# Performance work log

Measured on AMD Instinct MI355X. Metric: run time of the kernel, lower is better.

The kernel has to match this reference:

```python
import jax, jax.numpy as jnp
import numpy as np

B, T, NB, H = 1024, 128, 13, 128
T_IN = 64  # input_timesteps


def setup_inputs() -> dict:
    key = jax.random.key(0)
    ks = jax.random.split(key, 7)
    s = 1.0 / np.sqrt(H)
    return {
        "x": jax.random.normal(ks[0], (B, T, NB), dtype=jnp.float32),
        "W_ih": jax.random.normal(ks[1], (4 * H, NB), dtype=jnp.float32) * s,
        "W_hh": jax.random.normal(ks[2], (4 * H, H), dtype=jnp.float32) * s,
        "b_ih": jax.random.normal(ks[3], (4 * H,), dtype=jnp.float32) * s,
        "b_hh": jax.random.normal(ks[4], (4 * H,), dtype=jnp.float32) * s,
        "W_out": jax.random.normal(ks[5], (NB, H), dtype=jnp.float32) * s,
        "b_out": jax.random.normal(ks[6], (NB,), dtype=jnp.float32) * s,
    }


def _lstm_cell(x_t, h, c, W_ih, W_hh, b_ih, b_hh):
    # PyTorch nn.LSTM gate order: input, forget, cell(g), output
    gates = x_t @ W_ih.T + h @ W_hh.T + (b_ih + b_hh)  # [B, 4H]
    i, f, g, o = jnp.split(gates, 4, axis=-1)
    i = jax.nn.sigmoid(i)
    f = jax.nn.sigmoid(f)
    g = jnp.tanh(g)
    o = jax.nn.sigmoid(o)
    c_new = f * c + i * g
    h_new = o * jnp.tanh(c_new)
    return h_new, c_new


def reference(x, W_ih, W_hh, b_ih, b_hh, W_out, b_out):
    # forward_train with teacher_forcing=False, gp_enabled=False:
    # 1) teacher-fed LSTM over x[:, :T_IN]
    batch = x.shape[0]
    h0 = jnp.zeros((batch, H), dtype=x.dtype)
    c0 = jnp.zeros((batch, H), dtype=x.dtype)

    def step_teacher(carry, x_t):
        h, c = carry
        h, c = _lstm_cell(x_t, h, c, W_ih, W_hh, b_ih, b_hh)
        y = h @ W_out.T + b_out  # [B, NB]
        return (h, c), y

    (h, c), ys1 = jax.lax.scan(step_teacher, (h0, c0),
                               jnp.swapaxes(x[:, :T_IN], 0, 1))  # ys1: [T_IN, B, NB]

    remaining = T - T_IN - 1

    def step_auto(carry, _):
        h, c, inp = carry
        h, c = _lstm_cell(inp, h, c, W_ih, W_hh, b_ih, b_hh)
        y = h @ W_out.T + b_out
        return (h, c, y), y

    _, ys2 = jax.lax.scan(step_auto, (h, c, x[:, T_IN]), None, length=remaining)

    out = jnp.concatenate([
        x[:, 0:1],
        jnp.swapaxes(ys1, 0, 1),
        jnp.swapaxes(ys2, 0, 1),
    ], axis=1)  # [B, T, NB]
    return out
```

## Files before the change

### kernel.cpp

```cpp
#include <hip/hip_runtime.h>
#include <math.h>

#define BATCH 1024
#define TT    128
#define NBI   13
#define HH    128
#define T_INP 64
#define BB    4
#define NBLK  (BATCH/BB)

#define LOG2E 1.4426950408889634f
#define C2L   2.8853900817779268f
#define C4L   5.7707801635558537f

typedef _Float16 half8 __attribute__((ext_vector_type(8)));
typedef float    f32x4 __attribute__((ext_vector_type(4)));

__device__ __forceinline__ unsigned short f16b(float v) {
    return __builtin_bit_cast(unsigned short, (_Float16)v);
}
__device__ __forceinline__ float rcpf_(float x) { return __builtin_amdgcn_rcpf(x); }

#if __has_builtin(__builtin_amdgcn_exp2f)
__device__ __forceinline__ float exp2_(float x) { return __builtin_amdgcn_exp2f(x); }
#else
__device__ __forceinline__ float exp2_(float x) { return __expf(x * 0.6931471805599453f); }
#endif

__device__ __forceinline__ void barrier_lds() {
    asm volatile("s_waitcnt lgkmcnt(0)" ::: "memory");
    __builtin_amdgcn_sched_barrier(0);
    __builtin_amdgcn_s_barrier();
    __builtin_amdgcn_sched_barrier(0);
}

#define WS_WHH   0
#define WS_WHAT  131072
#define WS_WIHP  262144
#define WS_WOUT  294912
#define WS_BT    299008
#define WS_BA    301056

__global__ void fold_kernel(const float* __restrict__ W_ih,
                            const float* __restrict__ W_hh,
                            const float* __restrict__ b_ih,
                            const float* __restrict__ b_hh,
                            const float* __restrict__ W_out,
                            const float* __restrict__ b_out,
                            unsigned char* __restrict__ ws)
{
    const int j = blockIdx.x;
    const int k = threadIdx.x;
    unsigned short* whh16  = (unsigned short*)(ws + WS_WHH);
    unsigned short* what16 = (unsigned short*)(ws + WS_WHAT);
    unsigned short* wihp16 = (unsigned short*)(ws + WS_WIHP);
    unsigned short* wout16 = (unsigned short*)(ws + WS_WOUT);
    float* bias_t = (float*)(ws + WS_BT);
    float* bias_a = (float*)(ws + WS_BA);

    const int gate = j >> 7;
    const float sc = (gate == 2) ? (2.0f * LOG2E) : (-LOG2E);

    float whh = W_hh[j * HH + k];
    float acc = whh;
#pragma unroll
    for (int m = 0; m < NBI; ++m)
        acc += W_ih[j * NBI + m] * W_out[m * HH + k];
    whh16[j * HH + k]  = f16b(sc * whh);
    what16[j * HH + k] = f16b(sc * acc);

    if (k < 32) wihp16[j * 32 + k] = (k < NBI) ? f16b(sc * W_ih[j * NBI + k]) : (unsigned short)0;
    if (k == 0) {
        float bt = b_ih[j] + b_hh[j];
        bias_t[j] = sc * bt;
        float ba = bt;
#pragma unroll
        for (int m = 0; m < NBI; ++m) ba += W_ih[j * NBI + m] * b_out[m];
        bias_a[j] = sc * ba;
    }
    if (j < 16) wout16[j * HH + k] = (j < NBI) ? f16b(W_out[j * HH + k]) : (unsigned short)0;
}

#define MFMA16(A, B, C) __builtin_amdgcn_mfma_f32_16x16x32_f16((A), (B), (C), 0, 0, 0)

__global__ __launch_bounds__(512, 2)
void lstm_main(const float* __restrict__ x,
               const float* __restrict__ b_out,
               const unsigned char* __restrict__ ws,
               float* __restrict__ out)
{
    const int j  = threadIdx.x;
    const int w  = j >> 6;
    const int l  = j & 63;
    const int q  = l >> 4;
    const int cb = l & 15;
    const int bbase = blockIdx.x * BB;

    const unsigned short* whh16  = (const unsigned short*)(ws + WS_WHH);
    const unsigned short* what16 = (const unsigned short*)(ws + WS_WHAT);
    const unsigned short* wihp16 = (const unsigned short*)(ws + WS_WIHP);
    const unsigned short* wout16 = (const unsigned short*)(ws + WS_WOUT);
    const float* btfp = (const float*)(ws + WS_BT);
    const float* bafp = (const float*)(ws + WS_BA);

    __shared__ half8 h_s[2][16][16];
    __shared__ half8 x_s[2][4][16];
    __shared__ float g_sf[4 * 512];

    half8 wf[4][4];
    half8 wxf[4];
    half8 wof[4];
    f32x4 binit[4];
#pragma unroll
    for (int a = 0; a < 4; ++a) {
        const int row = 64 * w + 16 * a + cb;
#pragma unroll
        for (int kk = 0; kk < 4; ++kk)
            wf[a][kk] = *(const half8*)(whh16 + row * HH + 32 * kk + 8 * q);
        wxf[a] = *(const half8*)(wihp16 + row * 32 + 8 * q);
#pragma unroll
        for (int r = 0; r < 4; ++r)
            binit[a][r] = btfp[64 * w + 16 * a + 4 * q + r];
    }
    const bool projw = (w == 7);
#pragma unroll
    for (int kk = 0; kk < 4; ++kk)
        wof[kk] = *(const half8*)(wout16 + cb * HH + 32 * kk + 8 * q);

    f32x4 bo4;
#pragma unroll
    for (int r = 0; r < 4; ++r) {
        const int m = 4 * q + r;
        bo4[r] = (m < NBI) ? b_out[m] : 0.0f;
    }
    const f32x4 z4 = {0.f, 0.f, 0.f, 0.f};
    float* pob = out + (size_t)(bbase + (cb & 3)) * TT * NBI;

    const int uu = j & 127;
    const int ub = j >> 7;
    const float* gme = g_sf + ub * 512 + uu;

    const int  sid = j - 384;
    const bool stg = (sid >= 0) && (sid < 52);
    int s_b = 0, s_m = 0;
    const float* xp0 = x;
    float xa_h = 0.f;
    if (stg) { s_b = sid / 13; s_m = sid - 13 * s_b;
               xp0 = x + (size_t)(bbase + s_b) * TT * NBI + s_m; }

    ((half8*)h_s)[j] = (half8)(_Float16)0.0f;
    if (j < 128) ((half8*)x_s)[j] = (half8)(_Float16)0.0f;
    __syncthreads();
    if (stg) {
        float v = xp0[0];
        ((_Float16*)&x_s[0][s_m >> 3][s_b])[s_m & 7] = (_Float16)v;
        out[(size_t)(bbase + s_b) * TT * NBI + s_m] = v;
        xa_h = xp0[NBI];
    }
    __syncthreads();

    float c = 0.0f;
    int cur = 0;

    for (int t = 0; t <= T_INP; ++t) {
        const int nxt = cur ^ 1;

        float xa_p = 0.f;
        if (stg && t + 2 <= T_INP) xa_p = xp0[(t + 2) * NBI];

        half8 xf  = x_s[cur][q][cb];
        half8 hb0 = h_s[cur][q][cb];
        half8 hb1 = h_s[cur][4 + q][cb];
        half8 hb2 = h_s[cur][8 + q][cb];
        half8 hb3 = h_s[cur][12 + q][cb];

        f32x4 a0 = MFMA16(wxf[0], xf, binit[0]);
        f32x4 a1 = MFMA16(wxf[1], xf, binit[1]);
        f32x4 a2 = MFMA16(wxf[2], xf, binit[2]);
        f32x4 a3 = MFMA16(wxf[3], xf, binit[3]);
        a0 = MFMA16(wf[0][0], hb0, a0); a1 = MFMA16(wf[1][0], hb0, a1);
        a2 = MFMA16(wf[2][0], hb0, a2); a3 = MFMA16(wf[3][0], hb0, a3);
        a0 = MFMA16(wf[0][1], hb1, a0); a1 = MFMA16(wf[1][1], hb1, a1);
        a2 = MFMA16(wf[2][1], hb1, a2); a3 = MFMA16(wf[3][1], hb1, a3);
        a0 = MFMA16(wf[0][2], hb2, a0); a1 = MFMA16(wf[1][2], hb2, a1);
        a2 = MFMA16(wf[2][2], hb2, a2); a3 = MFMA16(wf[3][2], hb2, a3);
        a0 = MFMA16(wf[0][3], hb3, a0); a1 = MFMA16(wf[1][3], hb3, a1);
        a2 = MFMA16(wf[2][3], hb3, a2); a3 = MFMA16(wf[3][3], hb3, a3);

        f32x4 pacc = z4;
        if (projw) {
            pacc = MFMA16(wof[0], hb0, z4);
            pacc = MFMA16(wof[1], hb1, pacc);
            pacc = MFMA16(wof[2], hb2, pacc);
            pacc = MFMA16(wof[3], hb3, pacc);
        }

        if (cb < 4) {
            float* gb = g_sf + cb * 512 + 64 * w + 4 * q;
            *(f32x4*)(gb)      = a0;
            *(f32x4*)(gb + 16) = a1;
            *(f32x4*)(gb + 32) = a2;
            *(f32x4*)(gb + 48) = a3;
        }
        if (projw && t >= 1 && cb < 4) {
#pragma unroll
            for (int r = 0; r < 4; ++r) {
                const int m = 4 * q + r;
                if (m < NBI) pob[t * NBI + m] = pacc[r] + bo4[r];
            }
        }
        barrier_lds();

        {
            float gi = gme[0], gf = gme[128], gg = gme[256], go = gme[384];
            float ig = rcpf_(1.0f + exp2_(gi));
            float fg = rcpf_(1.0f + exp2_(gf));
            float rg = rcpf_(exp2_(gg) + 1.0f);
            float gp = C2L - C4L * rg;
            float og = rcpf_(1.0f + exp2_(go));
            float cn = fg * c + ig * gp;
            c = cn;
            float ec = exp2_(cn);
            float hv = og * (1.0f - 2.0f * rcpf_(ec + 1.0f));
            ((_Float16*)&h_s[nxt][uu >> 3][ub])[uu & 7] = (_Float16)hv;
        }
        if (stg && t + 1 <= T_INP) {
            ((_Float16*)&x_s[nxt][s_m >> 3][s_b])[s_m & 7] = (_Float16)xa_h;
            xa_h = xa_p;
        }
        barrier_lds();
        cur = nxt;
    }

#pragma unroll
    for (int a = 0; a < 4; ++a) {
        const int row = 64 * w + 16 * a + cb;
#pragma unroll
        for (int kk = 0; kk < 4; ++kk)
            wf[a][kk] = *(const half8*)(what16 + row * HH + 32 * kk + 8 * q);
#pragma unroll
        for (int r = 0; r < 4; ++r)
            binit[a][r] = bafp[64 * w + 16 * a + 4 * q + r];
    }

    for (int t = T_INP + 1; t < TT - 1; ++t) {
        const int nxt = cur ^ 1;

        half8 hb0 = h_s[cur][q][cb];
        half8 hb1 = h_s[cur][4 + q][cb];
        half8 hb2 = h_s[cur][8 + q][cb];
        half8 hb3 = h_s[cur][12 + q][cb];

        f32x4 a0 = MFMA16(wf[0][0], hb0, binit[0]);
        f32x4 a1 = MFMA16(wf[1][0], hb0, binit[1]);
        f32x4 a2 = MFMA16(wf[2][0], hb0, binit[2]);
        f32x4 a3 = MFMA16(wf[3][0], hb0, binit[3]);
        a0 = MFMA16(wf[0][1], hb1, a0); a1 = MFMA16(wf[1][1], hb1, a1);
        a2 = MFMA16(wf[2][1], hb1, a2); a3 = MFMA16(wf[3][1], hb1, a3);
        a0 = MFMA16(wf[0][2], hb2, a0); a1 = MFMA16(wf[1][2], hb2, a1);
        a2 = MFMA16(wf[2][2], hb2, a2); a3 = MFMA16(wf[3][2], hb2, a3);
        a0 = MFMA16(wf[0][3], hb3, a0); a1 = MFMA16(wf[1][3], hb3, a1);
        a2 = MFMA16(wf[2][3], hb3, a2); a3 = MFMA16(wf[3][3], hb3, a3);

        f32x4 pacc = z4;
        if (projw) {
            pacc = MFMA16(wof[0], hb0, z4);
            pacc = MFMA16(wof[1], hb1, pacc);
            pacc = MFMA16(wof[2], hb2, pacc);
            pacc = MFMA16(wof[3], hb3, pacc);
        }

        if (cb < 4) {
            float* gb = g_sf + cb * 512 + 64 * w + 4 * q;
            *(f32x4*)(gb)      = a0;
            *(f32x4*)(gb + 16) = a1;
            *(f32x4*)(gb + 32) = a2;
            *(f32x4*)(gb + 48) = a3;
        }
        if (projw && cb < 4) {
#pragma unroll
            for (int r = 0; r < 4; ++r) {
                const int m = 4 * q + r;
                if (m < NBI) pob[t * NBI + m] = pacc[r] + bo4[r];
            }
        }
        barrier_lds();

        {
            float gi = gme[0], gf = gme[128], gg = gme[256], go = gme[384];
            float ig = rcpf_(1.0f + exp2_(gi));
            float fg = rcpf_(1.0f + exp2_(gf));
            float rg = rcpf_(exp2_(gg) + 1.0f);
            float gp = C2L - C4L * rg;
            float og = rcpf_(1.0f + exp2_(go));
            float cn = fg * c + ig * gp;
            c = cn;
            float ec = exp2_(cn);
            float hv = og * (1.0f - 2.0f * rcpf_(ec + 1.0f));
            ((_Float16*)&h_s[nxt][uu >> 3][ub])[uu & 7] = (_Float16)hv;
        }
        barrier_lds();
        cur = nxt;
    }

    if (projw) {
        half8 hb0 = h_s[cur][q][cb];
        half8 hb1 = h_s[cur][4 + q][cb];
        half8 hb2 = h_s[cur][8 + q][cb];
        half8 hb3 = h_s[cur][12 + q][cb];
        f32x4 pacc = MFMA16(wof[0], hb0, z4);
        pacc = MFMA16(wof[1], hb1, pacc);
        pacc = MFMA16(wof[2], hb2, pacc);
        pacc = MFMA16(wof[3], hb3, pacc);
        if (cb < 4) {
#pragma unroll
            for (int r = 0; r < 4; ++r) {
                const int m = 4 * q + r;
                if (m < NBI) pob[(TT - 1) * NBI + m] = pacc[r] + bo4[r];
            }
        }
    }
}

extern "C" void kernel_launch(void* const* d_in, const int* in_sizes, int n_in,
                              void* d_out, int out_size, void* d_ws, size_t ws_size,
                              hipStream_t stream)
{
    const float* x     = (const float*)d_in[0];
    const float* W_ih  = (const float*)d_in[1];
    const float* W_hh  = (const float*)d_in[2];
    const float* b_ih  = (const float*)d_in[3];
    const float* b_hh  = (const float*)d_in[4];
    const float* W_out = (const float*)d_in[5];
    const float* b_out = (const float*)d_in[6];
    float* out = (float*)d_out;
    unsigned char* ws = (unsigned char*)d_ws;

    fold_kernel<<<512, HH, 0, stream>>>(W_ih, W_hh, b_ih, b_hh, W_out, b_out, ws);
    lstm_main<<<NBLK, 512, 0, stream>>>(x, b_out, ws, out);
}
```

Measured before the change: 179.9 us.

## Halve batch rows per block to double block count and occupancy

Each block now handles 2 batch rows instead of 4, so there are 512 blocks instead of 256, and launch bounds ask for 4 blocks per CU instead of 2. LDS arrays gain a padding column that all unused MFMA batch columns read from, and gate scratch rows are padded. Only the first 256 threads run the cell update. The aim is more parallelism across the 256 CUs on this latency-bound recurrence. The cost is that half of each MFMA's work is now wasted, and the tighter register budget from the higher occupancy target may cause spills, since each thread keeps about 24 half8 weight fragments in registers.

```diff
diff --git a/kernel.cpp b/kernel.cpp
--- a/kernel.cpp
+++ b/kernel.cpp
@@ -6,7 +6,7 @@
 #define NBI   13
 #define HH    128
 #define T_INP 64
-#define BB    4
+#define BB    2
 #define NBLK  (BATCH/BB)
 
 #define LOG2E 1.4426950408889634f
@@ -83,7 +83,7 @@
 
 #define MFMA16(A, B, C) __builtin_amdgcn_mfma_f32_16x16x32_f16((A), (B), (C), 0, 0, 0)
 
-__global__ __launch_bounds__(512, 2)
+__global__ __launch_bounds__(512, 4)
 void lstm_main(const float* __restrict__ x,
                const float* __restrict__ b_out,
                const unsigned char* __restrict__ ws,
@@ -103,9 +103,11 @@
     const float* btfp = (const float*)(ws + WS_BT);
     const float* bafp = (const float*)(ws + WS_BA);
 
-    __shared__ half8 h_s[2][16][16];
-    __shared__ half8 x_s[2][4][16];
-    __shared__ float g_sf[4 * 512];
+    __shared__ half8 h_s[2][16][17];
+    __shared__ half8 x_s[2][4][17];
+    __shared__ float g_sf[2 * 520];
+
+    const int cbn = (cb < BB) ? cb : 16;
 
     half8 wf[4][4];
     half8 wxf[4];
@@ -134,22 +136,27 @@
         bo4[r] = (m < NBI) ? b_out[m] : 0.0f;
     }
     const f32x4 z4 = {0.f, 0.f, 0.f, 0.f};
-    float* pob = out + (size_t)(bbase + (cb & 3)) * TT * NBI;
+    float* pob = out + (size_t)(bbase + (cb & 1)) * TT * NBI;
 
     const int uu = j & 127;
     const int ub = j >> 7;
-    const float* gme = g_sf + ub * 512 + uu;
+    const float* gme = g_sf + ub * 520 + uu;
 
     const int  sid = j - 384;
-    const bool stg = (sid >= 0) && (sid < 52);
+    const bool stg = (sid >= 0) && (sid < BB * NBI);
     int s_b = 0, s_m = 0;
     const float* xp0 = x;
     float xa_h = 0.f;
     if (stg) { s_b = sid / 13; s_m = sid - 13 * s_b;
                xp0 = x + (size_t)(bbase + s_b) * TT * NBI + s_m; }
 
-    ((half8*)h_s)[j] = (half8)(_Float16)0.0f;
-    if (j < 128) ((half8*)x_s)[j] = (half8)(_Float16)0.0f;
+    {
+        half8* hz = (half8*)h_s;
+        hz[j] = (half8)(_Float16)0.0f;
+        if (j < 32) hz[512 + j] = (half8)(_Float16)0.0f;
+        half8* xz = (half8*)x_s;
+        if (j < 136) xz[j] = (half8)(_Float16)0.0f;
+    }
     __syncthreads();
     if (stg) {
         float v = xp0[0];
@@ -168,11 +175,11 @@
         float xa_p = 0.f;
         if (stg && t + 2 <= T_INP) xa_p = xp0[(t + 2) * NBI];
 
-        half8 xf  = x_s[cur][q][cb];
-        half8 hb0 = h_s[cur][q][cb];
-        half8 hb1 = h_s[cur][4 + q][cb];
-        half8 hb2 = h_s[cur][8 + q][cb];
-        half8 hb3 = h_s[cur][12 + q][cb];
+        half8 xf  = x_s[cur][q][cbn];
+        half8 hb0 = h_s[cur][q][cbn];
+        half8 hb1 = h_s[cur][4 + q][cbn];
+        half8 hb2 = h_s[cur][8 + q][cbn];
+        half8 hb3 = h_s[cur][12 + q][cbn];
 
         f32x4 a0 = MFMA16(wxf[0], xf, binit[0]);
         f32x4 a1 = MFMA16(wxf[1], xf, binit[1]);
@@ -195,14 +202,14 @@
             pacc = MFMA16(wof[3], hb3, pacc);
         }
 
-        if (cb < 4) {
-            float* gb = g_sf + cb * 512 + 64 * w + 4 * q;
+        if (cb < BB) {
+            float* gb = g_sf + cb * 520 + 64 * w + 4 * q;
             *(f32x4*)(gb)      = a0;
             *(f32x4*)(gb + 16) = a1;
             *(f32x4*)(gb + 32) = a2;
             *(f32x4*)(gb + 48) = a3;
         }
-        if (projw && t >= 1 && cb < 4) {
+        if (projw && t >= 1 && cb < BB) {
 #pragma unroll
             for (int r = 0; r < 4; ++r) {
                 const int m = 4 * q + r;
@@ -211,7 +218,7 @@
         }
         barrier_lds();
 
-        {
+        if (j < 256) {
             float gi = gme[0], gf = gme[128], gg = gme[256], go = gme[384];
             float ig = rcpf_(1.0f + exp2_(gi));
             float fg = rcpf_(1.0f + exp2_(gf));
@@ -246,10 +253,10 @@
     for (int t = T_INP + 1; t < TT - 1; ++t) {
         const int nxt = cur ^ 1;
 
-        half8 hb0 = h_s[cur][q][cb];
-        half8 hb1 = h_s[cur][4 + q][cb];
-        half8 hb2 = h_s[cur][8 + q][cb];
-        half8 hb3 = h_s[cur][12 + q][cb];
+        half8 hb0 = h_s[cur][q][cbn];
+        half8 hb1 = h_s[cur][4 + q][cbn];
+        half8 hb2 = h_s[cur][8 + q][cbn];
+        half8 hb3 = h_s[cur][12 + q][cbn];
 
         f32x4 a0 = MFMA16(wf[0][0], hb0, binit[0]);
         f32x4 a1 = MFMA16(wf[1][0], hb0, binit[1]);
@@ -270,14 +277,14 @@
             pacc = MFMA16(wof[3], hb3, pacc);
         }
 
-        if (cb < 4) {
-            float* gb = g_sf + cb * 512 + 64 * w + 4 * q;
+        if (cb < BB) {
+            float* gb = g_sf + cb * 520 + 64 * w + 4 * q;
             *(f32x4*)(gb)      = a0;
             *(f32x4*)(gb + 16) = a1;
             *(f32x4*)(gb + 32) = a2;
             *(f32x4*)(gb + 48) = a3;
         }
-        if (projw && cb < 4) {
+        if (projw && cb < BB) {
 #pragma unroll
             for (int r = 0; r < 4; ++r) {
                 const int m = 4 * q + r;
@@ -286,7 +293,7 @@
         }
         barrier_lds();
 
-        {
+        if (j < 256) {
             float gi = gme[0], gf = gme[128], gg = gme[256], go = gme[384];
             float ig = rcpf_(1.0f + exp2_(gi));
             float fg = rcpf_(1.0f + exp2_(gf));
@@ -304,15 +311,15 @@
     }
 
     if (projw) {
-        half8 hb0 = h_s[cur][q][cb];
-        half8 hb1 = h_s[cur][4 + q][cb];
-        half8 hb2 = h_s[cur][8 + q][cb];
-        half8 hb3 = h_s[cur][12 + q][cb];
+        half8 hb0 = h_s[cur][q][cbn];
+        half8 hb1 = h_s[cur][4 + q][cbn];
+        half8 hb2 = h_s[cur][8 + q][cbn];
+        half8 hb3 = h_s[cur][12 + q][cbn];
         f32x4 pacc = MFMA16(wof[0], hb0, z4);
         pacc = MFMA16(wof[1], hb1, pacc);
         pacc = MFMA16(wof[2], hb2, pacc);
         pacc = MFMA16(wof[3], hb3, pacc);
-        if (cb < 4) {
+        if (cb < BB) {
 #pragma unroll
             for (int r = 0; r < 4; ++r) {
                 const int m = 4 * q + r;
```

New measurement: 424.0 us. +135.7%, slower.

## Split block batch into two interleaved chains to overlap MFMA with gate updates

Applied to the files above, without the earlier changes.

The 4 batch rows per block are split into two independent recurrent chains of 2 rows each, processed in alternating half-steps. While all waves run the MFMA gate matmul for one chain, half the threads apply the pointwise LSTM update for the other chain, so there is one barrier per half-step instead of a serial MFMA-then-update pair. This is meant to hide elementwise and LDS latency behind matrix work. In exchange, the MFMA count per row doubles because each 16-column tile now holds only 2 valid rows, and the padded LDS layout adds complexity.

```diff
diff --git a/kernel.cpp b/kernel.cpp
--- a/kernel.cpp
+++ b/kernel.cpp
@@ -83,6 +83,50 @@
 
 #define MFMA16(A, B, C) __builtin_amdgcn_mfma_f32_16x16x32_f16((A), (B), (C), 0, 0, 0)
 
+#define MFMA_HCHAIN() \
+    a0 = MFMA16(wf[0][0], hb0, a0); a1 = MFMA16(wf[1][0], hb0, a1); \
+    a2 = MFMA16(wf[2][0], hb0, a2); a3 = MFMA16(wf[3][0], hb0, a3); \
+    a0 = MFMA16(wf[0][1], hb1, a0); a1 = MFMA16(wf[1][1], hb1, a1); \
+    a2 = MFMA16(wf[2][1], hb1, a2); a3 = MFMA16(wf[3][1], hb1, a3); \
+    a0 = MFMA16(wf[0][2], hb2, a0); a1 = MFMA16(wf[1][2], hb2, a1); \
+    a2 = MFMA16(wf[2][2], hb2, a2); a3 = MFMA16(wf[3][2], hb2, a3); \
+    a0 = MFMA16(wf[0][3], hb3, a0); a1 = MFMA16(wf[1][3], hb3, a1); \
+    a2 = MFMA16(wf[2][3], hb3, a2); a3 = MFMA16(wf[3][3], hb3, a3);
+
+#define GATE_WRITE(CH) \
+    if (cb < 2) { \
+        float* gb = &g_sf[CH][cb * 520 + 64 * w + 4 * q]; \
+        *(f32x4*)(gb)      = a0; \
+        *(f32x4*)(gb + 16) = a1; \
+        *(f32x4*)(gb + 32) = a2; \
+        *(f32x4*)(gb + 48) = a3; \
+    }
+
+#define UPDATE(CH, PB) { \
+    float ig = rcpf_(1.0f + exp2_(gi)); \
+    float fg = rcpf_(1.0f + exp2_(gf)); \
+    float rg = rcpf_(exp2_(gg) + 1.0f); \
+    float gp = C2L - C4L * rg; \
+    float og = rcpf_(1.0f + exp2_(go)); \
+    float cn = fg * c + ig * gp; \
+    c = cn; \
+    float ec = exp2_(cn); \
+    float hv = og * (1.0f - 2.0f * rcpf_(ec + 1.0f)); \
+    ((_Float16*)&h_s[CH][PB][uu >> 3][ubb])[uu & 7] = (_Float16)hv; }
+
+#define PROJ4(STORE_T) { \
+    f32x4 pacc = MFMA16(wof[0], hb0, z4); \
+    pacc = MFMA16(wof[1], hb1, pacc); \
+    pacc = MFMA16(wof[2], hb2, pacc); \
+    pacc = MFMA16(wof[3], hb3, pacc); \
+    if (cb < 2) { \
+        _Pragma("unroll") \
+        for (int r = 0; r < 4; ++r) { \
+            const int m = 4 * q + r; \
+            if (m < NBI) pob[(STORE_T) * NBI + m] = pacc[r] + bo4[r]; \
+        } \
+    } }
+
 __global__ __launch_bounds__(512, 2)
 void lstm_main(const float* __restrict__ x,
                const float* __restrict__ b_out,
@@ -103,9 +147,11 @@
     const float* btfp = (const float*)(ws + WS_BT);
     const float* bafp = (const float*)(ws + WS_BA);
 
-    __shared__ half8 h_s[2][16][16];
-    __shared__ half8 x_s[2][4][16];
-    __shared__ float g_sf[4 * 512];
+    __shared__ half8 h_s[2][2][16][17];
+    __shared__ half8 x_s[2][2][4][17];
+    __shared__ float g_sf[2][2 * 520];
+
+    const int cbn = (cb < 2) ? cb : 16;
 
     half8 wf[4][4];
     half8 wxf[4];
@@ -122,7 +168,6 @@
         for (int r = 0; r < 4; ++r)
             binit[a][r] = btfp[64 * w + 16 * a + 4 * q + r];
     }
-    const bool projw = (w == 7);
 #pragma unroll
     for (int kk = 0; kk < 4; ++kk)
         wof[kk] = *(const half8*)(wout16 + cb * HH + 32 * kk + 8 * q);
@@ -134,102 +179,103 @@
         bo4[r] = (m < NBI) ? b_out[m] : 0.0f;
     }
     const f32x4 z4 = {0.f, 0.f, 0.f, 0.f};
-    float* pob = out + (size_t)(bbase + (cb & 3)) * TT * NBI;
-
-    const int uu = j & 127;
-    const int ub = j >> 7;
-    const float* gme = g_sf + ub * 512 + uu;
-
-    const int  sid = j - 384;
-    const bool stg = (sid >= 0) && (sid < 52);
+    float* pob = out + (size_t)(bbase + ((w == 7) ? 2 : 0) + (cb & 1)) * TT * NBI;
+
+    const int uchain = j >> 8;
+    const int uu  = j & 127;
+    const int ubb = (j >> 7) & 1;
+    const float* gme = g_sf[uchain] + ubb * 520 + uu;
+
+    const int sidA = j - 384, sidB = j - 416;
+    const bool stgA = (sidA >= 0) && (sidA < 26);
+    const bool stgB = (sidB >= 0) && (sidB < 26);
     int s_b = 0, s_m = 0;
     const float* xp0 = x;
-    float xa_h = 0.f;
-    if (stg) { s_b = sid / 13; s_m = sid - 13 * s_b;
-               xp0 = x + (size_t)(bbase + s_b) * TT * NBI + s_m; }
-
-    ((half8*)h_s)[j] = (half8)(_Float16)0.0f;
-    if (j < 128) ((half8*)x_s)[j] = (half8)(_Float16)0.0f;
+    float xh = 0.f, xp = 0.f;
+    if (stgA) { s_b = sidA / 13; s_m = sidA - 13 * s_b;
+                xp0 = x + (size_t)(bbase + s_b) * TT * NBI + s_m; }
+    if (stgB) { s_b = sidB / 13; s_m = sidB - 13 * s_b;
+                xp0 = x + (size_t)(bbase + 2 + s_b) * TT * NBI + s_m; }
+    const int schain = stgB ? 1 : 0;
+
+    {
+        half8* hz = (half8*)h_s;
+        hz[j] = (half8)(_Float16)0.0f;
+        hz[512 + j] = (half8)(_Float16)0.0f;
+        if (j < 64) hz[1024 + j] = (half8)(_Float16)0.0f;
+        half8* xz = (half8*)x_s;
+        if (j < 272) xz[j] = (half8)(_Float16)0.0f;
+    }
     __syncthreads();
-    if (stg) {
+    if (stgA || stgB) {
         float v = xp0[0];
-        ((_Float16*)&x_s[0][s_m >> 3][s_b])[s_m & 7] = (_Float16)v;
-        out[(size_t)(bbase + s_b) * TT * NBI + s_m] = v;
-        xa_h = xp0[NBI];
+        ((_Float16*)&x_s[schain][0][s_m >> 3][s_b])[s_m & 7] = (_Float16)v;
+        pobinit: ;
+        out[(size_t)(bbase + (stgB ? 2 : 0) + s_b) * TT * NBI + s_m] = v;
+        xh = xp0[NBI];
     }
     __syncthreads();
 
     float c = 0.0f;
-    int cur = 0;
+    int unused = 0; (void)unused;
 
     for (int t = 0; t <= T_INP; ++t) {
-        const int nxt = cur ^ 1;
-
-        float xa_p = 0.f;
-        if (stg && t + 2 <= T_INP) xa_p = xp0[(t + 2) * NBI];
-
-        half8 xf  = x_s[cur][q][cb];
-        half8 hb0 = h_s[cur][q][cb];
-        half8 hb1 = h_s[cur][4 + q][cb];
-        half8 hb2 = h_s[cur][8 + q][cb];
-        half8 hb3 = h_s[cur][12 + q][cb];
-
-        f32x4 a0 = MFMA16(wxf[0], xf, binit[0]);
-        f32x4 a1 = MFMA16(wxf[1], xf, binit[1]);
-        f32x4 a2 = MFMA16(wxf[2], xf, binit[2]);
-        f32x4 a3 = MFMA16(wxf[3], xf, binit[3]);
-        a0 = MFMA16(wf[0][0], hb0, a0); a1 = MFMA16(wf[1][0], hb0, a1);
-        a2 = MFMA16(wf[2][0], hb0, a2); a3 = MFMA16(wf[3][0], hb0, a3);
-        a0 = MFMA16(wf[0][1], hb1, a0); a1 = MFMA16(wf[1][1], hb1, a1);
-        a2 = MFMA16(wf[2][1], hb1, a2); a3 = MFMA16(wf[3][1], hb1, a3);
-        a0 = MFMA16(wf[0][2], hb2, a0); a1 = MFMA16(wf[1][2], hb2, a1);
-        a2 = MFMA16(wf[2][2], hb2, a2); a3 = MFMA16(wf[3][2], hb2, a3);
-        a0 = MFMA16(wf[0][3], hb3, a0); a1 = MFMA16(wf[1][3], hb3, a1);
-        a2 = MFMA16(wf[2][3], hb3, a2); a3 = MFMA16(wf[3][3], hb3, a3);
-
-        f32x4 pacc = z4;
-        if (projw) {
-            pacc = MFMA16(wof[0], hb0, z4);
-            pacc = MFMA16(wof[1], hb1, pacc);
-            pacc = MFMA16(wof[2], hb2, pacc);
-            pacc = MFMA16(wof[3], hb3, pacc);
-        }
-
-        if (cb < 4) {
-            float* gb = g_sf + cb * 512 + 64 * w + 4 * q;
-            *(f32x4*)(gb)      = a0;
-            *(f32x4*)(gb + 16) = a1;
-            *(f32x4*)(gb + 32) = a2;
-            *(f32x4*)(gb + 48) = a3;
-        }
-        if (projw && t >= 1 && cb < 4) {
-#pragma unroll
-            for (int r = 0; r < 4; ++r) {
-                const int m = 4 * q + r;
-                if (m < NBI) pob[t * NBI + m] = pacc[r] + bo4[r];
+        const int p  = t & 1;
+        const int pn = p ^ 1;
+
+        {
+            float gi = 0.f, gf = 0.f, gg = 0.f, go = 0.f;
+            const bool doU = (uchain == 1) && (t > 0);
+            if (doU) { gi = gme[0]; gf = gme[128]; gg = gme[256]; go = gme[384]; }
+            if (stgA && t + 2 <= T_INP) xp = xp0[(t + 2) * NBI];
+
+            half8 xf  = x_s[0][p][q][cbn];
+            half8 hb0 = h_s[0][p][q][cbn];
+            half8 hb1 = h_s[0][p][4 + q][cbn];
+            half8 hb2 = h_s[0][p][8 + q][cbn];
+            half8 hb3 = h_s[0][p][12 + q][cbn];
+
+            f32x4 a0 = MFMA16(wxf[0], xf, binit[0]);
+            f32x4 a1 = MFMA16(wxf[1], xf, binit[1]);
+            f32x4 a2 = MFMA16(wxf[2], xf, binit[2]);
+            f32x4 a3 = MFMA16(wxf[3], xf, binit[3]);
+            MFMA_HCHAIN();
+            GATE_WRITE(0);
+            if (w == 0 && t >= 1) PROJ4(t);
+            if (doU) UPDATE(1, p);
+            if (stgA && t + 1 <= T_INP) {
+                ((_Float16*)&x_s[0][pn][s_m >> 3][s_b])[s_m & 7] = (_Float16)xh;
+                xh = xp;
             }
-        }
-        barrier_lds();
+            barrier_lds();
+        }
 
         {
-            float gi = gme[0], gf = gme[128], gg = gme[256], go = gme[384];
-            float ig = rcpf_(1.0f + exp2_(gi));
-            float fg = rcpf_(1.0f + exp2_(gf));
-            float rg = rcpf_(exp2_(gg) + 1.0f);
-            float gp = C2L - C4L * rg;
-            float og = rcpf_(1.0f + exp2_(go));
-            float cn = fg * c + ig * gp;
-            c = cn;
-            float ec = exp2_(cn);
-            float hv = og * (1.0f - 2.0f * rcpf_(ec + 1.0f));
-            ((_Float16*)&h_s[nxt][uu >> 3][ub])[uu & 7] = (_Float16)hv;
-        }
-        if (stg && t + 1 <= T_INP) {
-            ((_Float16*)&x_s[nxt][s_m >> 3][s_b])[s_m & 7] = (_Float16)xa_h;
-            xa_h = xa_p;
-        }
-        barrier_lds();
-        cur = nxt;
+            float gi = 0.f, gf = 0.f, gg = 0.f, go = 0.f;
+            const bool doU = (uchain == 0);
+            if (doU) { gi = gme[0]; gf = gme[128]; gg = gme[256]; go = gme[384]; }
+            if (stgB && t + 2 <= T_INP) xp = xp0[(t + 2) * NBI];
+
+            half8 xf  = x_s[1][p][q][cbn];
+            half8 hb0 = h_s[1][p][q][cbn];
+            half8 hb1 = h_s[1][p][4 + q][cbn];
+            half8 hb2 = h_s[1][p][8 + q][cbn];
+            half8 hb3 = h_s[1][p][12 + q][cbn];
+
+            f32x4 a0 = MFMA16(wxf[0], xf, binit[0]);
+            f32x4 a1 = MFMA16(wxf[1], xf, binit[1]);
+            f32x4 a2 = MFMA16(wxf[2], xf, binit[2]);
+            f32x4 a3 = MFMA16(wxf[3], xf, binit[3]);
+            MFMA_HCHAIN();
+            GATE_WRITE(1);
+            if (w == 7 && t >= 1) PROJ4(t);
+            if (doU) UPDATE(0, pn);
+            if (stgB && t + 1 <= T_INP) {
+                ((_Float16*)&x_s[1][pn][s_m >> 3][s_b])[s_m & 7] = (_Float16)xh;
+                xh = xp;
+            }
+            barrier_lds();
+        }
     }
 
 #pragma unroll
@@ -244,81 +290,66 @@
     }
 
     for (int t = T_INP + 1; t < TT - 1; ++t) {
-        const int nxt = cur ^ 1;
-
-        half8 hb0 = h_s[cur][q][cb];
-        half8 hb1 = h_s[cur][4 + q][cb];
-        half8 hb2 = h_s[cur][8 + q][cb];
-        half8 hb3 = h_s[cur][12 + q][cb];
-
-        f32x4 a0 = MFMA16(wf[0][0], hb0, binit[0]);
-        f32x4 a1 = MFMA16(wf[1][0], hb0, binit[1]);
-        f32x4 a2 = MFMA16(wf[2][0], hb0, binit[2]);
-        f32x4 a3 = MFMA16(wf[3][0], hb0, binit[3]);
-        a0 = MFMA16(wf[0][1], hb1, a0); a1 = MFMA16(wf[1][1], hb1, a1);
-        a2 = MFMA16(wf[2][1], hb1, a2); a3 = MFMA16(wf[3][1], hb1, a3);
-        a0 = MFMA16(wf[0][2], hb2, a0); a1 = MFMA16(wf[1][2], hb2, a1);
-        a2 = MFMA16(wf[2][2], hb2, a2); a3 = MFMA16(wf[3][2], hb2, a3);
-        a0 = MFMA16(wf[0][3], hb3, a0); a1 = MFMA16(wf[1][3], hb3, a1);
-        a2 = MFMA16(wf[2][3], hb3, a2); a3 = MFMA16(wf[3][3], hb3, a3);
-
-        f32x4 pacc = z4;
-        if (projw) {
-            pacc = MFMA16(wof[0], hb0, z4);
-            pacc = MFMA16(wof[1], hb1, pacc);
-            pacc = MFMA16(wof[2], hb2, pacc);
-            pacc = MFMA16(wof[3], hb3, pacc);
-        }
-
-        if (cb < 4) {
-            float* gb = g_sf + cb * 512 + 64 * w + 4 * q;
-            *(f32x4*)(gb)      = a0;
-            *(f32x4*)(gb + 16) = a1;
-            *(f32x4*)(gb + 32) = a2;
-            *(f32x4*)(gb + 48) = a3;
-        }
-        if (projw && cb < 4) {
-#pragma unroll
-            for (int r = 0; r < 4; ++r) {
-                const int m = 4 * q + r;
-                if (m < NBI) pob[t * NBI + m] = pacc[r] + bo4[r];
-            }
-        }
+        const int p  = t & 1;
+        const int pn = p ^ 1;
+
+        {
+            float gi = 0.f, gf = 0.f, gg = 0.f, go = 0.f;
+            const bool doU = (uchain == 1);
+            if (doU) { gi = gme[0]; gf = gme[128]; gg = gme[256]; go = gme[384]; }
+
+            half8 hb0 = h_s[0][p][q][cbn];
+            half8 hb1 = h_s[0][p][4 + q][cbn];
+            half8 hb2 = h_s[0][p][8 + q][cbn];
+            half8 hb3 = h_s[0][p][12 + q][cbn];
+
+            f32x4 a0 = binit[0], a1 = binit[1], a2 = binit[2], a3 = binit[3];
+            MFMA_HCHAIN();
+            GATE_WRITE(0);
+            if (w == 0) PROJ4(t);
+            if (doU) UPDATE(1, p);
+            barrier_lds();
+        }
+
+        {
+            float gi = 0.f, gf = 0.f, gg = 0.f, go = 0.f;
+            const bool doU = (uchain == 0);
+            if (doU) { gi = gme[0]; gf = gme[128]; gg = gme[256]; go = gme[384]; }
+
+            half8 hb0 = h_s[1][p][q][cbn];
+            half8 hb1 = h_s[1][p][4 + q][cbn];
+            half8 hb2 = h_s[1][p][8 + q][cbn];
+            half8 hb3 = h_s[1][p][12 + q][cbn];
+
+            f32x4 a0 = binit[0], a1 = binit[1], a2 = binit[2], a3 = binit[3];
+            MFMA_HCHAIN();
+            GATE_WRITE(1);
+            if (w == 7) PROJ4(t);
+            if (doU) UPDATE(0, pn);
+            barrier_lds();
+        }
+    }
+
+    {
+        float gi = 0.f, gf = 0.f, gg = 0.f, go = 0.f;
+        const bool doU = (uchain == 1);
+        if (doU) { gi = gme[0]; gf = gme[128]; gg = gme[256]; go = gme[384]; }
+        if (w == 0) {
+            half8 hb0 = h_s[0][1][q][cbn];
+            half8 hb1 = h_s[0][1][4 + q][cbn];
+            half8 hb2 = h_s[0][1][8 + q][cbn];
+            half8 hb3 = h_s[0][1][12 + q][cbn];
+            PROJ4(TT - 1);
+        }
+        if (doU) UPDATE(1, 1);
         barrier_lds();
-
-        {
-            float gi = gme[0], gf = gme[128], gg = gme[256], go = gme[384];
-            float ig = rcpf_(1.0f + exp2_(gi));
-            float fg = rcpf_(1.0f + exp2_(gf));
-            float rg = rcpf_(exp2_(gg) + 1.0f);
-            float gp = C2L - C4L * rg;
-            float og = rcpf_(1.0f + exp2_(go));
-            float cn = fg * c + ig * gp;
-            c = cn;
-            float ec = exp2_(cn);
-            float hv = og * (1.0f - 2.0f * rcpf_(ec + 1.0f));
-            ((_Float16*)&h_s[nxt][uu >> 3][ub])[uu & 7] = (_Float16)hv;
-        }
-        barrier_lds();
-        cur = nxt;
-    }
-
-    if (projw) {
-        half8 hb0 = h_s[cur][q][cb];
-        half8 hb1 = h_s[cur][4 + q][cb];
-        half8 hb2 = h_s[cur][8 + q][cb];
-        half8 hb3 = h_s[cur][12 + q][cb];
-        f32x4 pacc = MFMA16(wof[0], hb0, z4);
-        pacc = MFMA16(wof[1], hb1, pacc);
-        pacc = MFMA16(wof[2], hb2, pacc);
-        pacc = MFMA16(wof[3], hb3, pacc);
-        if (cb < 4) {
-#pragma unroll
-            for (int r = 0; r < 4; ++r) {
-                const int m = 4 * q + r;
-                if (m < NBI) pob[(TT - 1) * NBI + m] = pacc[r] + bo4[r];
-            }
-        }
+    }
+    if (w == 7) {
+        half8 hb0 = h_s[1][1][q][cbn];
+        half8 hb1 = h_s[1][1][4 + q][cbn];
+        half8 hb2 = h_s[1][1][8 + q][cbn];
+        half8 hb3 = h_s[1][1][12 + q][cbn];
+        PROJ4(TT - 1);
     }
 }
 
```

Result: slower. 246.8 us (+37.2%).
